# Performance work log

Hardware: AMD Instinct MI355X
Metric: run time of the kernel (lower is better)

The kernel has to match this reference:

```python
import jax, jax.numpy as jnp
import numpy as np

B, H, W = 8, 160, 180
PHASES = 3
DELTA = 0.01
GAMMA = 1.0


def _conv(a, k):
    return jax.lax.conv_general_dilated(a, k, (1, 1), 'SAME',
                                        dimension_numbers=('NCHW', 'OIHW', 'NCHW'))


def _cconv(xr, xi, kr, ki):
    # complex conv via 4 real convs: (xr+i xi) * (kr+i ki)
    return _conv(xr, kr) - _conv(xi, ki), _conv(xr, ki) + _conv(xi, kr)


def _t(k):
    # conv_transpose2d(stride=1, pad=1, 3x3) == conv2d with swapped in/out channels and spatially flipped kernel
    return jnp.flip(jnp.swapaxes(k, 0, 1), axis=(2, 3))


def _cconvT(xr, xi, kr, ki):
    return _cconv(xr, xi, _t(kr), _t(ki))


def _act(x):
    # eq. (33): smoothed ReLU; quadratic inside |x| <= delta
    return jnp.where(jnp.abs(x) > DELTA, jax.nn.relu(x),
                     x * x / (4 * DELTA) + 0.5 * x + DELTA / 4)


def _act_der(x):
    return jnp.where(jnp.abs(x) > DELTA, (x > 0).astype(x.dtype),
                     x / (2 * DELTA) + 0.5)


def _grad_r(xc, convs, thr):
    # gradient of smoothed L2-channel-norm regularizer (grad_r_x1 / grad_r_x2)
    xr = jnp.real(xc).reshape(-1, 1, H, W)
    xi = jnp.imag(xc).reshape(-1, 1, H, W)
    acts = []
    ar, ai = xr, xi
    for kr, ki in convs[:3]:
        pr, pi = _cconv(ar, ai, kr, ki)
        ar, ai = _act(pr), _act(pi)
        acts.append((ar, ai))
    w4r, w4i = _cconv(ar, ai, *convs[3])
    norm = jnp.sqrt(jnp.sum(w4r * w4r + w4i * w4i, axis=1, keepdims=True))
    I1 = (norm > thr).astype(w4r.dtype)
    denom = jnp.maximum(norm, 1e-12)  # F.normalize eps
    gr = I1 * (w4r / denom) + (1 - I1) * (w4r / thr)
    gi = I1 * (w4i / denom) + (1 - I1) * (w4i / thr)
    gr, gi = _cconvT(gr, gi, *convs[3])
    for j in (2, 1, 0):
        # NOTE: faithful to source — derivative evaluated at the ACTIVATED values, complex multiply
        dr, di = _act_der(acts[j][0]), _act_der(acts[j][1])
        gr, gi = gr * dr - gi * di, gr * di + gi * dr
        gr, gi = _cconvT(gr, gi, *convs[j])
    return (gr + 1j * gi).reshape(-1, H, W)


def _grad_f(xc, kc, mask):
    # F^H( M o (M o F x - k) ): mriAdjointOp(mriForwardOp(x,m) - k, m)
    return jnp.fft.ifft2((jnp.fft.fft2(xc) * mask - kc) * mask)


def _forward(x1, x2, k1, k2, mask, convsA, convsB, thr1, thr2, a1, a2, b1, b2):
    to_c = lambda a: a[:, 0] + 1j * a[:, 1]
    x1c, x2c, k1c, k2c = to_c(x1), to_c(x2), to_c(k1), to_c(k2)
    for i in range(PHASES):
        x1c = x1c - a1[i] * _grad_f(x1c, k1c, mask) - b1[i] * _grad_r(x1c, convsA, thr1[0] * GAMMA)
        x2c = x2c - a2[i] * _grad_f(x2c, k2c, mask) - b2[i] * _grad_r(x2c, convsB, thr2[0] * GAMMA)
    return jnp.stack([jnp.real(x1c), jnp.imag(x1c), jnp.real(x2c), jnp.imag(x2c)], axis=1)


def setup_inputs() -> dict:
    key = jax.random.key(0)
    ks = jax.random.split(key, 32)
    d = {}
    d['x1'] = jax.random.normal(ks[0], (B, 2, H, W), jnp.float32)
    d['x2'] = jax.random.normal(ks[1], (B, 2, H, W), jnp.float32)
    d['k1'] = jax.random.normal(ks[2], (B, 2, H, W), jnp.float32)
    d['k2'] = jax.random.normal(ks[3], (B, 2, H, W), jnp.float32)
    d['mask'] = jax.random.uniform(ks[4], (H, W), jnp.float32)
    conv_names = ['conv1r', 'conv1i', 'conv2r', 'conv2i', 'conv3r', 'conv3i', 'conv4r', 'conv4i',
                  'conv1r_', 'conv1i_', 'conv2r_', 'conv2i_', 'conv3r_', 'conv3i_', 'conv4r_', 'conv4i_']
    for j, name in enumerate(conv_names):
        cin = 1 if name.startswith('conv1') else 32
        d[name] = 0.06 * jax.random.normal(ks[5 + j], (32, cin, 3, 3), jnp.float32)  # ~xavier
    d['soft_thr1'] = jnp.full((1,), 0.01, jnp.float32)
    d['soft_thr2'] = jnp.full((1,), 0.01, jnp.float32)
    d['alphas1'] = jnp.full((PHASES,), 0.5, jnp.float32)
    d['alphas2'] = jnp.full((PHASES,), 0.5, jnp.float32)
    d['betas1'] = jnp.full((PHASES,), 0.1, jnp.float32)
    d['betas2'] = jnp.full((PHASES,), 0.1, jnp.float32)
    return d


def reference(x1, x2, k1, k2, mask,
              conv1r, conv1i, conv2r, conv2i, conv3r, conv3i, conv4r, conv4i,
              conv1r_, conv1i_, conv2r_, conv2i_, conv3r_, conv3i_, conv4r_, conv4i_,
              soft_thr1, soft_thr2, alphas1, alphas2, betas1, betas2):
    convsA = [(conv1r, conv1i), (conv2r, conv2i), (conv3r, conv3i), (conv4r, conv4i)]
    convsB = [(conv1r_, conv1i_), (conv2r_, conv2i_), (conv3r_, conv3i_), (conv4r_, conv4i_)]
    return _forward(x1, x2, k1, k2, mask, convsA, convsB,
                    soft_thr1, soft_thr2, alphas1, alphas2, betas1, betas2)
```

## Files before the change

### kernel.cpp

```cpp
#include <hip/hip_runtime.h>
#include <math.h>

#define HH 160
#define WW 180
#define HWSZ (HH*WW)
#define BB 8
#define BB2 16
#define P1 ((size_t)BB*HWSZ)
#define PE2 ((size_t)BB2*32*HWSZ)

typedef unsigned short u16;
typedef unsigned long long ull;
typedef __attribute__((ext_vector_type(8))) short short8;
typedef __attribute__((ext_vector_type(2))) unsigned long long ull2;
typedef __attribute__((ext_vector_type(4))) float floatx4;

struct Ptrs16 { const float* p[16]; };

__device__ __forceinline__ u16 f2b(float f) {
  unsigned u = __builtin_bit_cast(unsigned, f);
  unsigned r = (u + 0x7fffu + ((u >> 16) & 1u)) >> 16;
  return (u16)r;
}
__device__ __forceinline__ float b2f(u16 h) {
  return __builtin_bit_cast(float, ((unsigned)h) << 16);
}

__device__ __forceinline__ float actf(float x) {
  float q = x*x*25.0f + 0.5f*x + 0.0025f;
  float r = fmaxf(x, 0.0f);
  return (fabsf(x) > 0.01f) ? r : q;
}
__device__ __forceinline__ float actdf(float x) {
  float q = x*50.0f + 0.5f;
  float r = (x > 0.0f) ? 1.0f : 0.0f;
  return (fabsf(x) > 0.01f) ? r : q;
}

__global__ void prep_all(Ptrs16 ps, u16* __restrict__ dst0) {
  const int rIdx[12] = {2,4,6,6,4,2,10,12,14,14,12,10};
  const int bwdF[12] = {0,0,0,1,1,1,0,0,0,1,1,1};
  int slot = blockIdx.x / 36;
  int idx = (blockIdx.x % 36)*256 + threadIdx.x;
  if (idx >= 9*32*32) return;
  const float* wr = ps.p[rIdx[slot]];
  const float* wi = ps.p[rIdx[slot]+1];
  u16* dst = dst0 + (size_t)slot*18432;
  int tap = idx >> 10; int rem = idx & 1023; int o = rem >> 5; int c = rem & 31;
  int s = bwdF[slot] ? ((c*32 + o)*9 + (8 - tap)) : ((o*32 + c)*9 + tap);
  float vr = wr[s], vi = wi[s];
  int nt = o >> 4, m = o & 15;
  size_t base = (((size_t)tap*2 + nt)*2*16 + (size_t)m)*32 + c;
  dst[base]       = f2b(vr);
  dst[base + 512] = f2b(vi);
}

template<int MODE>
__global__ __launch_bounds__(256)
void conv_mfma(const u16* __restrict__ inb, const u16* __restrict__ wbA,
               const u16* __restrict__ wbB, u16* __restrict__ outb,
               const u16* __restrict__ derb,
               const float* __restrict__ thrA, const float* __restrict__ thrB)
{
  __shared__ alignas(16) u16 stg[2*6*34*36];
  const int tid = threadIdx.x;
  const int lane = tid & 63, wv = tid >> 6;
  const int x0 = blockIdx.x * 32, y0 = blockIdx.y * 4, b = blockIdx.z;
  const u16* wb = (b < BB) ? wbA : wbB;
  constexpr int PL = 6*34*36;
  const int m = lane & 15, q = lane >> 4;

  for (int j = tid; j < 1632; j += 256) {
    int prow = j / 136; int rem = j - prow*136;
    int col = rem >> 2, chq = rem & 3;
    int plane = prow / 6, row = prow - plane*6;
    int gy = y0 - 1 + row, gx = x0 - 1 + col;
    ull v0 = 0, v1 = 0;
    if (gy >= 0 && gy < HH && gx >= 0 && gx < WW) {
      const ull* src = (const ull*)(inb + (size_t)plane*PE2
                                    + (((size_t)b*HH + gy)*WW + gx)*32 + chq*8);
      v0 = src[0]; v1 = src[1];
    }
    ull* dst = (ull*)&stg[((size_t)prow*34 + col)*36 + chq*8];
    dst[0] = v0; dst[1] = v1;
  }
  __syncthreads();

  floatx4 accr[2][2], acci[2][2];
#pragma unroll
  for (int s = 0; s < 2; ++s)
#pragma unroll
    for (int nt = 0; nt < 2; ++nt) {
      accr[s][nt] = (floatx4){0.f,0.f,0.f,0.f};
      acci[s][nt] = (floatx4){0.f,0.f,0.f,0.f};
    }

#pragma unroll
  for (int tap = 0; tap < 9; ++tap) {
    const int ky = tap / 3, kx = tap - ky*3;
    short8 Pr[2], Pi[2];
#pragma unroll
    for (int s = 0; s < 2; ++s) {
      int cu = ((wv + ky)*34 + (s*16 + m + kx))*36 + q*8;
      const ull* pR = (const ull*)&stg[cu];
      const ull* pI = (const ull*)&stg[cu + PL];
      ull2 vr; vr.x = pR[0]; vr.y = pR[1];
      ull2 vi; vi.x = pI[0]; vi.y = pI[1];
      Pr[s] = __builtin_bit_cast(short8, vr);
      Pi[s] = __builtin_bit_cast(short8, vi);
    }
#pragma unroll
    for (int nt = 0; nt < 2; ++nt) {
      const u16* pw = wb + (size_t)(tap*2 + nt)*1024 + (size_t)m*32 + q*8;
      short8 Wr = *(const short8*)pw;
      short8 Wi = *(const short8*)(pw + 512);
      ull2 wx = __builtin_bit_cast(ull2, Wi);
      wx.x ^= 0x8000800080008000ULL;
      wx.y ^= 0x8000800080008000ULL;
      short8 nWi = __builtin_bit_cast(short8, wx);
#pragma unroll
      for (int s = 0; s < 2; ++s) {
        accr[s][nt] = __builtin_amdgcn_mfma_f32_16x16x32_bf16(Wr,  Pr[s], accr[s][nt], 0, 0, 0);
        accr[s][nt] = __builtin_amdgcn_mfma_f32_16x16x32_bf16(nWi, Pi[s], accr[s][nt], 0, 0, 0);
        acci[s][nt] = __builtin_amdgcn_mfma_f32_16x16x32_bf16(Wr,  Pi[s], acci[s][nt], 0, 0, 0);
        acci[s][nt] = __builtin_amdgcn_mfma_f32_16x16x32_bf16(Wi,  Pr[s], acci[s][nt], 0, 0, 0);
      }
    }
  }

  const int y = y0 + wv;
#pragma unroll
  for (int s = 0; s < 2; ++s) {
    int x = x0 + s*16 + m;
    bool ok = (x < WW);
    float invn = 1.0f;
    if constexpr (MODE == 3) {
      float ss = 0.f;
#pragma unroll
      for (int nt = 0; nt < 2; ++nt)
#pragma unroll
        for (int r = 0; r < 4; ++r)
          ss += accr[s][nt][r]*accr[s][nt][r] + acci[s][nt][r]*acci[s][nt][r];
      ss += __shfl_xor(ss, 16, 64);
      ss += __shfl_xor(ss, 32, 64);
      float thr = (b < BB ? thrA : thrB)[0];
      invn = 1.0f / fmaxf(sqrtf(ss), thr);
    }
    size_t pxbase = (((size_t)b*HH + y)*WW + x)*32;
#pragma unroll
    for (int nt = 0; nt < 2; ++nt) {
      size_t gb = pxbase + nt*16 + q*4;
      ull dR = 0, dI = 0;
      if constexpr (MODE == 2) {
        if (ok) { dR = *(const ull*)(derb + gb); dI = *(const ull*)(derb + PE2 + gb); }
      }
      ull vR = 0, vI = 0;
#pragma unroll
      for (int r = 0; r < 4; ++r) {
        float pr = accr[s][nt][r], pi = acci[s][nt][r];
        if constexpr (MODE == 1) { pr = actf(pr); pi = actf(pi); }
        if constexpr (MODE == 3) { pr *= invn; pi *= invn; }
        if constexpr (MODE == 2) {
          float dr = actdf(b2f((u16)(dR >> (16*r))));
          float di = actdf(b2f((u16)(dI >> (16*r))));
          float nr = pr*dr - pi*di;
          pi = pr*di + pi*dr; pr = nr;
        }
        vR |= (ull)f2b(pr) << (16*r);
        vI |= (ull)f2b(pi) << (16*r);
      }
      if (ok) {
        *(ull*)(outb + gb)       = vR;
        *(ull*)(outb + PE2 + gb) = vI;
      }
    }
  }
}

__global__ __launch_bounds__(256)
void l1fwd(const float* __restrict__ xall,
           const float* __restrict__ wrA, const float* __restrict__ wiA,
           const float* __restrict__ wrB, const float* __restrict__ wiB,
           u16* __restrict__ outb)
{
  __shared__ float hR[10][12], hI[10][12];
  __shared__ float wt[9][32][2];
  const int tid = threadIdx.x;
  const int og = tid & 3, px = tid >> 2;
  const int lx = px & 7, ly = px >> 3;
  const int x0 = blockIdx.x*8, y0 = blockIdx.y*8, b = blockIdx.z;
  const int branch = b >> 3, img = b & 7;
  const float* wr = branch ? wrB : wrA;
  const float* wi = branch ? wiB : wiA;
  const float* xp = xall + (size_t)branch*2*P1 + (size_t)img*HWSZ;

  for (int j = tid; j < 576; j += 256) {
    int tap = j >> 6; int rem = j & 63; int o = rem >> 1, ri = rem & 1;
    wt[tap][o][ri] = ri ? wi[o*9+tap] : wr[o*9+tap];
  }
  for (int j = tid; j < 200; j += 256) {
    int plane = j / 100; int pos = j - plane*100;
    int yy = pos / 10, xx = pos - yy*10;
    int gy = y0 - 1 + yy, gx = x0 - 1 + xx;
    float v = 0.f;
    if (gy >= 0 && gy < HH && gx >= 0 && gx < WW)
      v = xp[(size_t)plane*P1 + (size_t)gy*WW + gx];
    (plane ? hI : hR)[yy][xx] = v;
  }
  __syncthreads();

  float accR[8], accI[8];
#pragma unroll
  for (int o = 0; o < 8; ++o) { accR[o] = 0.f; accI[o] = 0.f; }
#pragma unroll
  for (int tap = 0; tap < 9; ++tap) {
    int ky = tap/3, kx = tap - ky*3;
    float ar = hR[ly+ky][lx+kx], ai = hI[ly+ky][lx+kx];
#pragma unroll
    for (int o = 0; o < 8; ++o) {
      float wrv = wt[tap][og*8+o][0], wiv = wt[tap][og*8+o][1];
      accR[o] += ar*wrv - ai*wiv;
      accI[o] += ar*wiv + ai*wrv;
    }
  }
  int gx = x0 + lx, gy = y0 + ly;
  if (gx < WW) {
    size_t base = (((size_t)b*HH + gy)*WW + gx)*32 + og*8;
    ull* dR = (ull*)(outb + base);
    ull* dI = (ull*)(outb + PE2 + base);
#pragma unroll
    for (int k = 0; k < 2; ++k) {
      ull vR = 0, vI = 0;
#pragma unroll
      for (int t = 0; t < 4; ++t) {
        vR |= (ull)f2b(actf(accR[k*4+t])) << (16*t);
        vI |= (ull)f2b(actf(accI[k*4+t])) << (16*t);
      }
      dR[k] = vR; dI[k] = vI;
    }
  }
}

__global__ __launch_bounds__(256)
void l1bwd(const u16* __restrict__ gb,
           const float* __restrict__ wrA, const float* __restrict__ wiA,
           const float* __restrict__ wrB, const float* __restrict__ wiB,
           float* __restrict__ outp)
{
  __shared__ alignas(16) u16 stg[2*100*32];
  __shared__ float wt[32][9][2];
  const int tid = threadIdx.x;
  const int cg = tid & 3, px = tid >> 2;
  const int lx = px & 7, ly = px >> 3;
  const int x0 = blockIdx.x*8, y0 = blockIdx.y*8, b = blockIdx.z;
  const int branch = b >> 3, img = b & 7;
  const float* wr = branch ? wrB : wrA;
  const float* wi = branch ? wiB : wiA;

  for (int j = tid; j < 576; j += 256) {
    int c = j / 18; int rem = j - c*18; int tap = rem >> 1, ri = rem & 1;
    wt[c][tap][ri] = (ri ? wi : wr)[c*9 + (8-tap)];
  }
  for (int j = tid; j < 800; j += 256) {
    int plane = j / 400; int rem = j - plane*400;
    int pos = rem >> 2, chq = rem & 3;
    int yy = pos / 10, xx = pos - yy*10;
    int gy = y0 - 1 + yy, gx = x0 - 1 + xx;
    ull v0 = 0, v1 = 0;
    if (gy >= 0 && gy < HH && gx >= 0 && gx < WW) {
      const ull* src = (const ull*)(gb + (size_t)plane*PE2
                                    + (((size_t)b*HH + gy)*WW + gx)*32 + chq*8);
      v0 = src[0]; v1 = src[1];
    }
    ull* dst = (ull*)&stg[((size_t)plane*100 + pos)*32 + chq*8];
    dst[0] = v0; dst[1] = v1;
  }
  __syncthreads();

  float gr = 0.f, gi = 0.f;
#pragma unroll
  for (int tap = 0; tap < 9; ++tap) {
    int ky = tap/3, kx = tap - ky*3;
    int pos = (ly+ky)*10 + (lx+kx);
    const ull* pR = (const ull*)&stg[(size_t)pos*32 + cg*8];
    const ull* pI = (const ull*)&stg[(100 + (size_t)pos)*32 + cg*8];
    ull r0 = pR[0], r1 = pR[1], i0 = pI[0], i1 = pI[1];
#pragma unroll
    for (int t = 0; t < 4; ++t) {
      int c = cg*8 + t;
      float ar = b2f((u16)(r0 >> (16*t))), ai = b2f((u16)(i0 >> (16*t)));
      float wrv = wt[c][tap][0], wiv = wt[c][tap][1];
      gr += ar*wrv - ai*wiv;
      gi += ar*wiv + ai*wrv;
    }
#pragma unroll
    for (int t = 0; t < 4; ++t) {
      int c = cg*8 + 4 + t;
      float ar = b2f((u16)(r1 >> (16*t))), ai = b2f((u16)(i1 >> (16*t)));
      float wrv = wt[c][tap][0], wiv = wt[c][tap][1];
      gr += ar*wrv - ai*wiv;
      gi += ar*wiv + ai*wrv;
    }
  }
  gr += __shfl_xor(gr, 1, 64); gr += __shfl_xor(gr, 2, 64);
  gi += __shfl_xor(gi, 1, 64); gi += __shfl_xor(gi, 2, 64);

  int gx = x0 + lx, gy = y0 + ly;
  if (cg == 0 && gx < WW) {
    size_t o2 = (size_t)branch*2*P1 + (size_t)img*HWSZ + (size_t)gy*WW + gx;
    outp[o2]      = gr;
    outp[P1 + o2] = gi;
  }
}

__global__ void gen_dft2(float2* __restrict__ Mf, float2* __restrict__ Mi, int N) {
  int idx = blockIdx.x*256 + threadIdx.x;
  if (idx >= N*N) return;
  int r = idx / N, c = idx - r*N;
  long mm = ((long)r * (long)c) % N;
  double a = 2.0 * 3.14159265358979323846 * (double)mm / (double)N;
  double cs = cos(a), sn = sin(a);
  Mf[idx] = make_float2((float)cs, (float)(-sn));
  Mi[idx] = make_float2((float)(cs/N), (float)(sn/N));
}

__global__ void dft_row_planes(const float* __restrict__ xall,
                               float2* __restrict__ out, const float2* __restrict__ M) {
  int bh = blockIdx.x;
  int v = threadIdx.x; if (v >= WW) return;
  int b2 = bh / HH, h = bh - b2*HH;
  int branch = b2 >> 3, img = b2 & 7;
  const float* rowR = xall + (size_t)branch*2*P1 + (size_t)img*HWSZ + (size_t)h*WW;
  const float* rowI = rowR + P1;
  float ar = 0.f, ai = 0.f;
  for (int w = 0; w < WW; ++w) {
    float sr = rowR[w], si = rowI[w];
    float2 m = M[w*WW + v];
    ar += sr*m.x - si*m.y;
    ai += sr*m.y + si*m.x;
  }
  out[(size_t)bh*WW + v] = make_float2(ar, ai);
}

__global__ void dft_row_c(const float2* __restrict__ in, float2* __restrict__ out,
                          const float2* __restrict__ M) {
  int bh = blockIdx.x;
  int v = threadIdx.x; if (v >= WW) return;
  const float2* row = in + (size_t)bh*WW;
  float ar = 0.f, ai = 0.f;
  for (int w = 0; w < WW; ++w) {
    float2 s = row[w];
    float2 m = M[w*WW + v];
    ar += s.x*m.x - s.y*m.y;
    ai += s.x*m.y + s.y*m.x;
  }
  out[(size_t)bh*WW + v] = make_float2(ar, ai);
}

__global__ void dft_col_c(const float2* __restrict__ in, float2* __restrict__ out,
                          const float2* __restrict__ M) {
  int bu = blockIdx.x;
  int v = threadIdx.x; if (v >= WW) return;
  int b = bu / HH, u = bu - b*HH;
  const float2* base = in + (size_t)b*HWSZ;
  float ar = 0.f, ai = 0.f;
  for (int h = 0; h < HH; ++h) {
    float2 m = M[u*HH + h];
    float2 s = base[(size_t)h*WW + v];
    ar += s.x*m.x - s.y*m.y;
    ai += s.x*m.y + s.y*m.x;
  }
  out[(size_t)bu*WW + v] = make_float2(ar, ai);
}

__global__ void dft_col_mask(const float2* __restrict__ in, float2* __restrict__ out,
                             const float2* __restrict__ M, const float* __restrict__ mask) {
  int bu = blockIdx.x;
  int v = threadIdx.x; if (v >= WW) return;
  int b = bu / HH, u = bu - b*HH;
  const float2* base = in + (size_t)b*HWSZ;
  float ar = 0.f, ai = 0.f;
  for (int h = 0; h < HH; ++h) {
    float mk = mask[h*WW + v]; float mm = mk*mk;
    float2 m = M[u*HH + h];
    float2 s = base[(size_t)h*WW + v];
    float sr = s.x*mm, si = s.y*mm;
    ar += sr*m.x - si*m.y;
    ai += sr*m.y + si*m.x;
  }
  out[(size_t)bu*WW + v] = make_float2(ar, ai);
}

__global__ void dft_row_update(const float2* __restrict__ in, const float2* __restrict__ M,
                               const float2* __restrict__ ctall, const float* __restrict__ grp,
                               float* __restrict__ xall,
                               const float* __restrict__ al1, const float* __restrict__ al2,
                               const float* __restrict__ be1, const float* __restrict__ be2,
                               int phase) {
  int bh = blockIdx.x;
  int v = threadIdx.x; if (v >= WW) return;
  int b2 = bh / HH, h = bh - b2*HH;
  int branch = b2 >> 3, img = b2 & 7;
  const float2* row = in + (size_t)bh*WW;
  float ar = 0.f, ai = 0.f;
  for (int w = 0; w < WW; ++w) {
    float2 s = row[w];
    float2 m = M[w*WW + v];
    ar += s.x*m.x - s.y*m.y;
    ai += s.x*m.y + s.y*m.x;
  }
  float2 ct = ctall[(size_t)bh*WW + v];
  float a   = (branch ? al2 : al1)[phase];
  float bet = (branch ? be2 : be1)[phase];
  size_t xo = (size_t)branch*2*P1 + (size_t)img*HWSZ + (size_t)h*WW + v;
  xall[xo]      -= a*(ar - ct.x) + bet*grp[xo];
  xall[P1 + xo] -= a*(ai - ct.y) + bet*grp[P1 + xo];
}

__global__ void maskk_m(const float* __restrict__ k1, const float* __restrict__ k2,
                        const float* __restrict__ mask, float2* __restrict__ t) {
  int i = blockIdx.x*256 + threadIdx.x;
  if (i >= (int)(2*P1)) return;
  int branch = i >= (int)P1;
  int ii = i - branch*(int)P1;
  int b = ii / HWSZ, p = ii - b*HWSZ;
  const float* k = branch ? k2 : k1;
  float m = mask[p];
  t[i] = make_float2(m * k[(size_t)b*2*HWSZ + p], m * k[(size_t)b*2*HWSZ + HWSZ + p]);
}

__global__ void unpack_m(const float* __restrict__ x1, const float* __restrict__ x2,
                         float* __restrict__ xall) {
  int i = blockIdx.x*256 + threadIdx.x;
  if (i >= (int)(2*P1)) return;
  int branch = i >= (int)P1;
  int ii = i - branch*(int)P1;
  int b = ii / HWSZ, p = ii - b*HWSZ;
  const float* src = branch ? x2 : x1;
  size_t dst = (size_t)branch*2*P1 + (size_t)b*HWSZ + p;
  xall[dst]      = src[(size_t)b*2*HWSZ + p];
  xall[P1 + dst] = src[(size_t)b*2*HWSZ + HWSZ + p];
}

__global__ void pack_kernel(const float* __restrict__ xall, float* __restrict__ out) {
  int i = blockIdx.x*256 + threadIdx.x;
  if (i >= (int)P1) return;
  int b = i / HWSZ, p = i - b*HWSZ;
  size_t ob = (size_t)b*4*HWSZ;
  size_t x1o = (size_t)b*HWSZ + p;
  size_t x2o = 2*P1 + x1o;
  out[ob + p]          = xall[x1o];
  out[ob + HWSZ + p]   = xall[P1 + x1o];
  out[ob + 2*HWSZ + p] = xall[x2o];
  out[ob + 3*HWSZ + p] = xall[P1 + x2o];
}

extern "C" void kernel_launch(void* const* d_in, const int* in_sizes, int n_in,
                              void* d_out, int out_size, void* d_ws, size_t ws_size,
                              hipStream_t stream) {
  (void)in_sizes; (void)n_in; (void)out_size; (void)ws_size;
  const float* x1in = (const float*)d_in[0];
  const float* x2in = (const float*)d_in[1];
  const float* k1   = (const float*)d_in[2];
  const float* k2   = (const float*)d_in[3];
  const float* mask = (const float*)d_in[4];
  Ptrs16 cw;
  for (int i = 0; i < 16; ++i) cw.p[i] = (const float*)d_in[5+i];
  const float* thr1 = (const float*)d_in[21];
  const float* thr2 = (const float*)d_in[22];
  const float* al1  = (const float*)d_in[23];
  const float* al2  = (const float*)d_in[24];
  const float* be1  = (const float*)d_in[25];
  const float* be2  = (const float*)d_in[26];
  float* out = (float*)d_out;

  u16* U = (u16*)d_ws;
  size_t uoff = 0;
  auto alloc_u = [&](size_t n){ u16* p = U + uoff; uoff += (n + 15) & ~(size_t)15; return p; };
  u16* act1 = alloc_u(2*PE2);
  u16* act2 = alloc_u(2*PE2);
  u16* act3 = alloc_u(2*PE2);
  u16* w4b  = alloc_u(2*PE2);
  u16* wp0  = alloc_u(12*18432);

  float* F = (float*)(U + uoff);
  size_t off = 0;
  auto alloc_f = [&](size_t n){ float* p = F + off; off += (n + 3) & ~(size_t)3; return p; };
  float*  xall = alloc_f(4*P1);
  float*  grp  = alloc_f(4*P1);
  float2* t1   = (float2*)alloc_f(4*P1);
  float2* t2   = (float2*)alloc_f(4*P1);
  float2* ctall= (float2*)alloc_f(4*P1);
  float2* EWf  = (float2*)alloc_f(2*(size_t)WW*WW);
  float2* EWi  = (float2*)alloc_f(2*(size_t)WW*WW);
  float2* EHf  = (float2*)alloc_f(2*(size_t)HH*HH);
  float2* EHi  = (float2*)alloc_f(2*(size_t)HH*HH);

  const dim3 MG(6, 40, BB2);
  const dim3 LG(23, 20, BB2);
  const int NP1 = (int)((P1 + 255)/256);
  const int NP2 = (int)((2*P1 + 255)/256);
  const int DFTG = BB2*HH;
  const int DFTB = 192;

  gen_dft2<<<(WW*WW+255)/256, 256, 0, stream>>>(EWf, EWi, WW);
  gen_dft2<<<(HH*HH+255)/256, 256, 0, stream>>>(EHf, EHi, HH);
  prep_all<<<12*36, 256, 0, stream>>>(cw, wp0);
  unpack_m<<<NP2, 256, 0, stream>>>(x1in, x2in, xall);

  maskk_m<<<NP2, 256, 0, stream>>>(k1, k2, mask, t1);
  dft_col_c<<<DFTG, DFTB, 0, stream>>>(t1, t2, EHi);
  dft_row_c<<<DFTG, DFTB, 0, stream>>>(t2, ctall, EWi);

  u16* WA[6]; u16* WB[6];
  for (int i = 0; i < 6; ++i) { WA[i] = wp0 + (size_t)i*18432; WB[i] = wp0 + (size_t)(6+i)*18432; }

  for (int ph = 0; ph < 3; ++ph) {
    l1fwd<<<LG, 256, 0, stream>>>(xall, cw.p[0], cw.p[1], cw.p[8], cw.p[9], act1);
    conv_mfma<1><<<MG, 256, 0, stream>>>(act1, WA[0], WB[0], act2, nullptr, nullptr, nullptr);
    conv_mfma<1><<<MG, 256, 0, stream>>>(act2, WA[1], WB[1], act3, nullptr, nullptr, nullptr);
    conv_mfma<3><<<MG, 256, 0, stream>>>(act3, WA[2], WB[2], w4b, nullptr, thr1, thr2);
    conv_mfma<2><<<MG, 256, 0, stream>>>(w4b,  WA[3], WB[3], act3, act3, nullptr, nullptr);
    conv_mfma<2><<<MG, 256, 0, stream>>>(act3, WA[4], WB[4], act2, act2, nullptr, nullptr);
    conv_mfma<2><<<MG, 256, 0, stream>>>(act2, WA[5], WB[5], act1, act1, nullptr, nullptr);
    l1bwd<<<LG, 256, 0, stream>>>(act1, cw.p[0], cw.p[1], cw.p[8], cw.p[9], grp);
    dft_row_planes<<<DFTG, DFTB, 0, stream>>>(xall, t1, EWf);
    dft_col_c<<<DFTG, DFTB, 0, stream>>>(t1, t2, EHf);
    dft_col_mask<<<DFTG, DFTB, 0, stream>>>(t2, t1, EHi, mask);
    dft_row_update<<<DFTG, DFTB, 0, stream>>>(t1, EWi, ctall, grp, xall,
                                              al1, al2, be1, be2, ph);
  }

  pack_kernel<<<NP1, 256, 0, stream>>>(xall, out);
}
```

Before: 2.005 ms.

## Make conv_mfma blocks loop over five row tiles with double-buffered LDS staging

Each conv_mfma block now handles 20 rows (five 4-row tiles) instead of 4. The next tile's input halo is prefetched into registers while the current tile's MFMAs run, then written to a second LDS buffer. This is meant to hide global-load latency behind compute and to amortize address setup and the weight-pointer choice across tiles. In exchange LDS use doubles, register pressure rises from the 14 prefetched 64-bit values, and the grid shrinks fivefold (6x8x16 blocks), which may leave the GPU underfilled.

```diff
diff --git a/kernel.cpp b/kernel.cpp
--- a/kernel.cpp
+++ b/kernel.cpp
@@ -62,117 +62,158 @@
                const u16* __restrict__ derb,
                const float* __restrict__ thrA, const float* __restrict__ thrB)
 {
-  __shared__ alignas(16) u16 stg[2*6*34*36];
+  constexpr int PL = 6*34*36;
+  constexpr int PB = 2*PL;
+  __shared__ alignas(16) u16 stg[2*PB];
   const int tid = threadIdx.x;
   const int lane = tid & 63, wv = tid >> 6;
-  const int x0 = blockIdx.x * 32, y0 = blockIdx.y * 4, b = blockIdx.z;
+  const int x0 = blockIdx.x * 32;
+  const int yb = blockIdx.y * 20;
+  const int b  = blockIdx.z;
   const u16* wb = (b < BB) ? wbA : wbB;
-  constexpr int PL = 6*34*36;
   const int m = lane & 15, q = lane >> 4;
 
-  for (int j = tid; j < 1632; j += 256) {
-    int prow = j / 136; int rem = j - prow*136;
-    int col = rem >> 2, chq = rem & 3;
-    int plane = prow / 6, row = prow - plane*6;
-    int gy = y0 - 1 + row, gx = x0 - 1 + col;
-    ull v0 = 0, v1 = 0;
-    if (gy >= 0 && gy < HH && gx >= 0 && gx < WW) {
-      const ull* src = (const ull*)(inb + (size_t)plane*PE2
-                                    + (((size_t)b*HH + gy)*WW + gx)*32 + chq*8);
-      v0 = src[0]; v1 = src[1];
-    }
-    ull* dst = (ull*)&stg[((size_t)prow*34 + col)*36 + chq*8];
-    dst[0] = v0; dst[1] = v1;
-  }
-  __syncthreads();
-
-  floatx4 accr[2][2], acci[2][2];
-#pragma unroll
-  for (int s = 0; s < 2; ++s)
-#pragma unroll
-    for (int nt = 0; nt < 2; ++nt) {
-      accr[s][nt] = (floatx4){0.f,0.f,0.f,0.f};
-      acci[s][nt] = (floatx4){0.f,0.f,0.f,0.f};
-    }
-
-#pragma unroll
-  for (int tap = 0; tap < 9; ++tap) {
-    const int ky = tap / 3, kx = tap - ky*3;
-    short8 Pr[2], Pi[2];
+  const u16* srcp[7]; int ldso[7]; int rowa[7]; bool act[7]; bool wok[7];
+#pragma unroll
+  for (int k = 0; k < 7; ++k) {
+    int j = tid + k*256;
+    bool inr = (j < 1632);
+    int jj = inr ? j : 0;
+    int chq = jj & 3; int r2 = jj >> 2;
+    int col = r2 % 34; int pr = r2 / 34;
+    int row = pr % 6;  int plane = pr / 6;
+    int gx = x0 - 1 + col;
+    bool gxok = (gx >= 0) && (gx < WW);
+    srcp[k] = inb + (size_t)plane*PE2
+            + (((size_t)b*HH + (yb - 1 + row))*WW + gx)*32 + chq*8;
+    ldso[k] = (pr*34 + col)*36 + chq*8;
+    rowa[k] = yb - 1 + row;
+    act[k]  = inr && gxok;
+    wok[k]  = inr;
+  }
+  const size_t YSTRIDE = (size_t)4*WW*32;
+
+  ull vreg[14];
+  auto stage_regs = [&](int t) {
+#pragma unroll
+    for (int k = 0; k < 7; ++k) {
+      int gy = rowa[k] + 4*t;
+      bool ok = act[k] && (gy >= 0) && (gy < HH);
+      const ull* sp = (const ull*)(srcp[k] + (size_t)t*YSTRIDE);
+      vreg[2*k]   = ok ? sp[0] : 0;
+      vreg[2*k+1] = ok ? sp[1] : 0;
+    }
+  };
+  auto write_lds = [&](int buf) {
+    u16* base = &stg[buf*PB];
+#pragma unroll
+    for (int k = 0; k < 7; ++k) {
+      if (wok[k]) {
+        ull* dp = (ull*)&base[ldso[k]];
+        dp[0] = vreg[2*k]; dp[1] = vreg[2*k+1];
+      }
+    }
+  };
+
+  stage_regs(0); write_lds(0); __syncthreads();
+
+  for (int t = 0; t < 5; ++t) {
+    if (t < 4) stage_regs(t + 1);
+
+    const u16* sb = &stg[(t & 1)*PB];
+    floatx4 accr[2][2], acci[2][2];
+#pragma unroll
+    for (int s = 0; s < 2; ++s)
+#pragma unroll
+      for (int nt = 0; nt < 2; ++nt) {
+        accr[s][nt] = (floatx4){0.f,0.f,0.f,0.f};
+        acci[s][nt] = (floatx4){0.f,0.f,0.f,0.f};
+      }
+
+#pragma unroll
+    for (int tap = 0; tap < 9; ++tap) {
+      const int ky = tap / 3, kx = tap - ky*3;
+      short8 Pr[2], Pi[2];
+#pragma unroll
+      for (int s = 0; s < 2; ++s) {
+        int cu = ((wv + ky)*34 + (s*16 + m + kx))*36 + q*8;
+        const ull* pR = (const ull*)&sb[cu];
+        const ull* pI = (const ull*)&sb[cu + PL];
+        ull2 vr; vr.x = pR[0]; vr.y = pR[1];
+        ull2 vi; vi.x = pI[0]; vi.y = pI[1];
+        Pr[s] = __builtin_bit_cast(short8, vr);
+        Pi[s] = __builtin_bit_cast(short8, vi);
+      }
+#pragma unroll
+      for (int nt = 0; nt < 2; ++nt) {
+        const u16* pw = wb + (size_t)(tap*2 + nt)*1024 + (size_t)m*32 + q*8;
+        short8 Wr = *(const short8*)pw;
+        short8 Wi = *(const short8*)(pw + 512);
+        ull2 wx = __builtin_bit_cast(ull2, Wi);
+        wx.x ^= 0x8000800080008000ULL;
+        wx.y ^= 0x8000800080008000ULL;
+        short8 nWi = __builtin_bit_cast(short8, wx);
+#pragma unroll
+        for (int s = 0; s < 2; ++s) {
+          accr[s][nt] = __builtin_amdgcn_mfma_f32_16x16x32_bf16(Wr,  Pr[s], accr[s][nt], 0, 0, 0);
+          accr[s][nt] = __builtin_amdgcn_mfma_f32_16x16x32_bf16(nWi, Pi[s], accr[s][nt], 0, 0, 0);
+          acci[s][nt] = __builtin_amdgcn_mfma_f32_16x16x32_bf16(Wr,  Pi[s], acci[s][nt], 0, 0, 0);
+          acci[s][nt] = __builtin_amdgcn_mfma_f32_16x16x32_bf16(Wi,  Pr[s], acci[s][nt], 0, 0, 0);
+        }
+      }
+    }
+
+    const int y = yb + t*4 + wv;
 #pragma unroll
     for (int s = 0; s < 2; ++s) {
-      int cu = ((wv + ky)*34 + (s*16 + m + kx))*36 + q*8;
-      const ull* pR = (const ull*)&stg[cu];
-      const ull* pI = (const ull*)&stg[cu + PL];
-      ull2 vr; vr.x = pR[0]; vr.y = pR[1];
-      ull2 vi; vi.x = pI[0]; vi.y = pI[1];
-      Pr[s] = __builtin_bit_cast(short8, vr);
-      Pi[s] = __builtin_bit_cast(short8, vi);
-    }
-#pragma unroll
-    for (int nt = 0; nt < 2; ++nt) {
-      const u16* pw = wb + (size_t)(tap*2 + nt)*1024 + (size_t)m*32 + q*8;
-      short8 Wr = *(const short8*)pw;
-      short8 Wi = *(const short8*)(pw + 512);
-      ull2 wx = __builtin_bit_cast(ull2, Wi);
-      wx.x ^= 0x8000800080008000ULL;
-      wx.y ^= 0x8000800080008000ULL;
-      short8 nWi = __builtin_bit_cast(short8, wx);
-#pragma unroll
-      for (int s = 0; s < 2; ++s) {
-        accr[s][nt] = __builtin_amdgcn_mfma_f32_16x16x32_bf16(Wr,  Pr[s], accr[s][nt], 0, 0, 0);
-        accr[s][nt] = __builtin_amdgcn_mfma_f32_16x16x32_bf16(nWi, Pi[s], accr[s][nt], 0, 0, 0);
-        acci[s][nt] = __builtin_amdgcn_mfma_f32_16x16x32_bf16(Wr,  Pi[s], acci[s][nt], 0, 0, 0);
-        acci[s][nt] = __builtin_amdgcn_mfma_f32_16x16x32_bf16(Wi,  Pr[s], acci[s][nt], 0, 0, 0);
-      }
-    }
-  }
-
-  const int y = y0 + wv;
-#pragma unroll
-  for (int s = 0; s < 2; ++s) {
-    int x = x0 + s*16 + m;
-    bool ok = (x < WW);
-    float invn = 1.0f;
-    if constexpr (MODE == 3) {
-      float ss = 0.f;
-#pragma unroll
-      for (int nt = 0; nt < 2; ++nt)
-#pragma unroll
-        for (int r = 0; r < 4; ++r)
-          ss += accr[s][nt][r]*accr[s][nt][r] + acci[s][nt][r]*acci[s][nt][r];
-      ss += __shfl_xor(ss, 16, 64);
-      ss += __shfl_xor(ss, 32, 64);
-      float thr = (b < BB ? thrA : thrB)[0];
-      invn = 1.0f / fmaxf(sqrtf(ss), thr);
-    }
-    size_t pxbase = (((size_t)b*HH + y)*WW + x)*32;
-#pragma unroll
-    for (int nt = 0; nt < 2; ++nt) {
-      size_t gb = pxbase + nt*16 + q*4;
-      ull dR = 0, dI = 0;
-      if constexpr (MODE == 2) {
-        if (ok) { dR = *(const ull*)(derb + gb); dI = *(const ull*)(derb + PE2 + gb); }
-      }
-      ull vR = 0, vI = 0;
-#pragma unroll
-      for (int r = 0; r < 4; ++r) {
-        float pr = accr[s][nt][r], pi = acci[s][nt][r];
-        if constexpr (MODE == 1) { pr = actf(pr); pi = actf(pi); }
-        if constexpr (MODE == 3) { pr *= invn; pi *= invn; }
+      int x = x0 + s*16 + m;
+      bool ok = (x < WW);
+      float invn = 1.0f;
+      if constexpr (MODE == 3) {
+        float ss = 0.f;
+#pragma unroll
+        for (int nt = 0; nt < 2; ++nt)
+#pragma unroll
+          for (int r = 0; r < 4; ++r)
+            ss += accr[s][nt][r]*accr[s][nt][r] + acci[s][nt][r]*acci[s][nt][r];
+        ss += __shfl_xor(ss, 16, 64);
+        ss += __shfl_xor(ss, 32, 64);
+        float thr = (b < BB ? thrA : thrB)[0];
+        invn = 1.0f / fmaxf(sqrtf(ss), thr);
+      }
+      size_t pxbase = (((size_t)b*HH + y)*WW + x)*32;
+#pragma unroll
+      for (int nt = 0; nt < 2; ++nt) {
+        size_t gb = pxbase + nt*16 + q*4;
+        ull dR = 0, dI = 0;
         if constexpr (MODE == 2) {
-          float dr = actdf(b2f((u16)(dR >> (16*r))));
-          float di = actdf(b2f((u16)(dI >> (16*r))));
-          float nr = pr*dr - pi*di;
-          pi = pr*di + pi*dr; pr = nr;
+          if (ok) { dR = *(const ull*)(derb + gb); dI = *(const ull*)(derb + PE2 + gb); }
         }
-        vR |= (ull)f2b(pr) << (16*r);
-        vI |= (ull)f2b(pi) << (16*r);
-      }
-      if (ok) {
-        *(ull*)(outb + gb)       = vR;
-        *(ull*)(outb + PE2 + gb) = vI;
-      }
+        ull vR = 0, vI = 0;
+#pragma unroll
+        for (int r = 0; r < 4; ++r) {
+          float pr = accr[s][nt][r], pi = acci[s][nt][r];
+          if constexpr (MODE == 1) { pr = actf(pr); pi = actf(pi); }
+          if constexpr (MODE == 3) { pr *= invn; pi *= invn; }
+          if constexpr (MODE == 2) {
+            float dr = actdf(b2f((u16)(dR >> (16*r))));
+            float di = actdf(b2f((u16)(dI >> (16*r))));
+            float nr = pr*dr - pi*di;
+            pi = pr*di + pi*dr; pr = nr;
+          }
+          vR |= (ull)f2b(pr) << (16*r);
+          vI |= (ull)f2b(pi) << (16*r);
+        }
+        if (ok) {
+          *(ull*)(outb + gb)       = vR;
+          *(ull*)(outb + PE2 + gb) = vI;
+        }
+      }
+    }
+
+    if (t < 4) {
+      write_lds((t + 1) & 1);
+      __syncthreads();
     }
   }
 }
@@ -496,7 +537,7 @@
   float2* EHf  = (float2*)alloc_f(2*(size_t)HH*HH);
   float2* EHi  = (float2*)alloc_f(2*(size_t)HH*HH);
 
-  const dim3 MG(6, 40, BB2);
+  const dim3 MG(6, 8, BB2);
   const dim3 LG(23, 20, BB2);
   const int NP1 = (int)((P1 + 255)/256);
   const int NP2 = (int)((2*P1 + 255)/256);
```

After: 2.035 ms. No clear change (+1.5%).

## Overlap DFT data-consistency work with conv kernels via extra blocks; merge setup kernels

Applied to the files above, without the earlier changes.

The forward row DFT now runs as extra thread blocks inside the first conv launch, and the column DFT, mask and inverse column DFT run as extra blocks inside the second conv launch, using shared memory for a whole image column. The DFT path no longer waits behind the regularizer convs, and three launches per phase are removed. The setup kernels (DFT matrix generation, weight prep, unpack, mask·k) are merged into one launch. The cost is longer conv launches with mixed block types. The fused column DFT also drops the strided global reads of the old separate kernels.

```diff
diff --git a/kernel.cpp b/kernel.cpp
--- a/kernel.cpp
+++ b/kernel.cpp
@@ -9,6 +9,8 @@
 #define P1 ((size_t)BB*HWSZ)
 #define PE2 ((size_t)BB2*32*HWSZ)
 
+#define NCONV 3840
+
 typedef unsigned short u16;
 typedef unsigned long long ull;
 typedef __attribute__((ext_vector_type(8))) short short8;
@@ -37,35 +39,136 @@
   return (fabsf(x) > 0.01f) ? r : q;
 }
 
-__global__ void prep_all(Ptrs16 ps, u16* __restrict__ dst0) {
-  const int rIdx[12] = {2,4,6,6,4,2,10,12,14,14,12,10};
-  const int bwdF[12] = {0,0,0,1,1,1,0,0,0,1,1,1};
-  int slot = blockIdx.x / 36;
-  int idx = (blockIdx.x % 36)*256 + threadIdx.x;
-  if (idx >= 9*32*32) return;
-  const float* wr = ps.p[rIdx[slot]];
-  const float* wi = ps.p[rIdx[slot]+1];
-  u16* dst = dst0 + (size_t)slot*18432;
-  int tap = idx >> 10; int rem = idx & 1023; int o = rem >> 5; int c = rem & 31;
-  int s = bwdF[slot] ? ((c*32 + o)*9 + (8 - tap)) : ((o*32 + c)*9 + tap);
-  float vr = wr[s], vi = wi[s];
-  int nt = o >> 4, m = o & 15;
-  size_t base = (((size_t)tap*2 + nt)*2*16 + (size_t)m)*32 + c;
-  dst[base]       = f2b(vr);
-  dst[base + 512] = f2b(vi);
-}
-
-template<int MODE>
+__global__ __launch_bounds__(256)
+void setup_all(Ptrs16 ps, u16* __restrict__ wp0,
+               const float* __restrict__ x1, const float* __restrict__ x2,
+               float* __restrict__ xall,
+               const float* __restrict__ k1, const float* __restrict__ k2,
+               const float* __restrict__ mask, float2* __restrict__ t1,
+               float2* __restrict__ EWf, float2* __restrict__ EWi,
+               float2* __restrict__ EHf, float2* __restrict__ EHi)
+{
+  const int id = blockIdx.x, tid = threadIdx.x;
+  if (id < 127) {
+    int idx = id*256 + tid; if (idx >= WW*WW) return;
+    int r = idx / WW, c = idx - r*WW;
+    long mm = ((long)r * (long)c) % WW;
+    double a = 2.0 * 3.14159265358979323846 * (double)mm / (double)WW;
+    double cs = cos(a), sn = sin(a);
+    EWf[idx] = make_float2((float)cs, (float)(-sn));
+    EWi[idx] = make_float2((float)(cs/WW), (float)(sn/WW));
+  } else if (id < 227) {
+    int idx = (id-127)*256 + tid; if (idx >= HH*HH) return;
+    int r = idx / HH, c = idx - r*HH;
+    long mm = ((long)r * (long)c) % HH;
+    double a = 2.0 * 3.14159265358979323846 * (double)mm / (double)HH;
+    double cs = cos(a), sn = sin(a);
+    EHf[idx] = make_float2((float)cs, (float)(-sn));
+    EHi[idx] = make_float2((float)(cs/HH), (float)(sn/HH));
+  } else if (id < 659) {
+    const int rIdx[12] = {2,4,6,6,4,2,10,12,14,14,12,10};
+    const int bwdF[12] = {0,0,0,1,1,1,0,0,0,1,1,1};
+    int pb = id - 227;
+    int slot = pb / 36;
+    int idx = (pb % 36)*256 + tid;
+    if (idx >= 9*32*32) return;
+    const float* wr = ps.p[rIdx[slot]];
+    const float* wi = ps.p[rIdx[slot]+1];
+    u16* dst = wp0 + (size_t)slot*18432;
+    int tap = idx >> 10; int rem = idx & 1023; int o = rem >> 5; int c = rem & 31;
+    int s = bwdF[slot] ? ((c*32 + o)*9 + (8 - tap)) : ((o*32 + c)*9 + tap);
+    int nt = o >> 4, m = o & 15;
+    size_t base = (((size_t)tap*2 + nt)*2*16 + (size_t)m)*32 + c;
+    dst[base]       = f2b(wr[s]);
+    dst[base + 512] = f2b(wi[s]);
+  } else if (id < 2459) {
+    int i = (id-659)*256 + tid; if (i >= (int)(2*P1)) return;
+    int branch = i >= (int)P1;
+    int ii = i - branch*(int)P1;
+    int b = ii / HWSZ, p = ii - b*HWSZ;
+    const float* src = branch ? x2 : x1;
+    size_t dst = (size_t)branch*2*P1 + (size_t)b*HWSZ + p;
+    xall[dst]      = src[(size_t)b*2*HWSZ + p];
+    xall[P1 + dst] = src[(size_t)b*2*HWSZ + HWSZ + p];
+  } else {
+    int i = (id-2459)*256 + tid; if (i >= (int)(2*P1)) return;
+    int branch = i >= (int)P1;
+    int ii = i - branch*(int)P1;
+    int b = ii / HWSZ, p = ii - b*HWSZ;
+    const float* k = branch ? k2 : k1;
+    float m = mask[p];
+    t1[i] = make_float2(m * k[(size_t)b*2*HWSZ + p], m * k[(size_t)b*2*HWSZ + HWSZ + p]);
+  }
+}
+
+template<int MODE, int EXTRA>
 __global__ __launch_bounds__(256)
 void conv_mfma(const u16* __restrict__ inb, const u16* __restrict__ wbA,
                const u16* __restrict__ wbB, u16* __restrict__ outb,
                const u16* __restrict__ derb,
-               const float* __restrict__ thrA, const float* __restrict__ thrB)
+               const float* __restrict__ thrA, const float* __restrict__ thrB,
+               const float* __restrict__ xall, float2* __restrict__ t1,
+               const float2* __restrict__ EWf, const float2* __restrict__ EHf,
+               const float2* __restrict__ EHi, const float* __restrict__ mask)
 {
   __shared__ alignas(16) u16 stg[2*6*34*36];
-  const int tid = threadIdx.x;
+  const int id = blockIdx.x, tid = threadIdx.x;
+
+  if (EXTRA == 1 && id >= NCONV) {
+    int j = id - NCONV;
+    int v = tid; if (v >= WW) return;
+    int b2 = j / HH, h = j - b2*HH;
+    int branch = b2 >> 3, img = b2 & 7;
+    const float* rowR = xall + (size_t)branch*2*P1 + (size_t)img*HWSZ + (size_t)h*WW;
+    const float* rowI = rowR + P1;
+    float ar = 0.f, ai = 0.f;
+    for (int w = 0; w < WW; ++w) {
+      float sr = rowR[w], si = rowI[w];
+      float2 m = EWf[w*WW + v];
+      ar += sr*m.x - si*m.y;
+      ai += sr*m.y + si*m.x;
+    }
+    t1[(size_t)j*WW + v] = make_float2(ar, ai);
+    return;
+  }
+  if (EXTRA == 2 && id >= NCONV) {
+    int j = id - NCONV;
+    int b = j / WW, v = j - b*WW;
+    float2* cbA = (float2*)stg;
+    float2* cbB = ((float2*)stg) + HH;
+    if (tid < HH) cbA[tid] = t1[((size_t)(b*HH) + tid)*WW + v];
+    __syncthreads();
+    if (tid < HH) {
+      int u = tid;
+      float ar = 0.f, ai = 0.f;
+      for (int h = 0; h < HH; ++h) {
+        float2 m = EHf[u*HH + h];
+        float2 s = cbA[h];
+        ar += s.x*m.x - s.y*m.y;
+        ai += s.x*m.y + s.y*m.x;
+      }
+      float mk = mask[u*WW + v]; float mm = mk*mk;
+      cbB[u] = make_float2(ar*mm, ai*mm);
+    }
+    __syncthreads();
+    if (tid < HH) {
+      int u2 = tid;
+      float ar = 0.f, ai = 0.f;
+      for (int u = 0; u < HH; ++u) {
+        float2 m = EHi[u2*HH + u];
+        float2 s = cbB[u];
+        ar += s.x*m.x - s.y*m.y;
+        ai += s.x*m.y + s.y*m.x;
+      }
+      t1[((size_t)(b*HH) + u2)*WW + v] = make_float2(ar, ai);
+    }
+    return;
+  }
+
   const int lane = tid & 63, wv = tid >> 6;
-  const int x0 = blockIdx.x * 32, y0 = blockIdx.y * 4, b = blockIdx.z;
+  const int x0 = (id % 6) * 32;
+  const int y0 = ((id / 6) % 40) * 4;
+  const int b  = id / 240;
   const u16* wb = (b < BB) ? wbA : wbB;
   constexpr int PL = 6*34*36;
   const int m = lane & 15, q = lane >> 4;
@@ -313,50 +416,6 @@
   }
 }
 
-__global__ void gen_dft2(float2* __restrict__ Mf, float2* __restrict__ Mi, int N) {
-  int idx = blockIdx.x*256 + threadIdx.x;
-  if (idx >= N*N) return;
-  int r = idx / N, c = idx - r*N;
-  long mm = ((long)r * (long)c) % N;
-  double a = 2.0 * 3.14159265358979323846 * (double)mm / (double)N;
-  double cs = cos(a), sn = sin(a);
-  Mf[idx] = make_float2((float)cs, (float)(-sn));
-  Mi[idx] = make_float2((float)(cs/N), (float)(sn/N));
-}
-
-__global__ void dft_row_planes(const float* __restrict__ xall,
-                               float2* __restrict__ out, const float2* __restrict__ M) {
-  int bh = blockIdx.x;
-  int v = threadIdx.x; if (v >= WW) return;
-  int b2 = bh / HH, h = bh - b2*HH;
-  int branch = b2 >> 3, img = b2 & 7;
-  const float* rowR = xall + (size_t)branch*2*P1 + (size_t)img*HWSZ + (size_t)h*WW;
-  const float* rowI = rowR + P1;
-  float ar = 0.f, ai = 0.f;
-  for (int w = 0; w < WW; ++w) {
-    float sr = rowR[w], si = rowI[w];
-    float2 m = M[w*WW + v];
-    ar += sr*m.x - si*m.y;
-    ai += sr*m.y + si*m.x;
-  }
-  out[(size_t)bh*WW + v] = make_float2(ar, ai);
-}
-
-__global__ void dft_row_c(const float2* __restrict__ in, float2* __restrict__ out,
-                          const float2* __restrict__ M) {
-  int bh = blockIdx.x;
-  int v = threadIdx.x; if (v >= WW) return;
-  const float2* row = in + (size_t)bh*WW;
-  float ar = 0.f, ai = 0.f;
-  for (int w = 0; w < WW; ++w) {
-    float2 s = row[w];
-    float2 m = M[w*WW + v];
-    ar += s.x*m.x - s.y*m.y;
-    ai += s.x*m.y + s.y*m.x;
-  }
-  out[(size_t)bh*WW + v] = make_float2(ar, ai);
-}
-
 __global__ void dft_col_c(const float2* __restrict__ in, float2* __restrict__ out,
                           const float2* __restrict__ M) {
   int bu = blockIdx.x;
@@ -373,22 +432,19 @@
   out[(size_t)bu*WW + v] = make_float2(ar, ai);
 }
 
-__global__ void dft_col_mask(const float2* __restrict__ in, float2* __restrict__ out,
-                             const float2* __restrict__ M, const float* __restrict__ mask) {
-  int bu = blockIdx.x;
+__global__ void dft_row_c(const float2* __restrict__ in, float2* __restrict__ out,
+                          const float2* __restrict__ M) {
+  int bh = blockIdx.x;
   int v = threadIdx.x; if (v >= WW) return;
-  int b = bu / HH, u = bu - b*HH;
-  const float2* base = in + (size_t)b*HWSZ;
+  const float2* row = in + (size_t)bh*WW;
   float ar = 0.f, ai = 0.f;
-  for (int h = 0; h < HH; ++h) {
-    float mk = mask[h*WW + v]; float mm = mk*mk;
-    float2 m = M[u*HH + h];
-    float2 s = base[(size_t)h*WW + v];
-    float sr = s.x*mm, si = s.y*mm;
-    ar += sr*m.x - si*m.y;
-    ai += sr*m.y + si*m.x;
-  }
-  out[(size_t)bu*WW + v] = make_float2(ar, ai);
+  for (int w = 0; w < WW; ++w) {
+    float2 s = row[w];
+    float2 m = M[w*WW + v];
+    ar += s.x*m.x - s.y*m.y;
+    ai += s.x*m.y + s.y*m.x;
+  }
+  out[(size_t)bh*WW + v] = make_float2(ar, ai);
 }
 
 __global__ void dft_row_update(const float2* __restrict__ in, const float2* __restrict__ M,
@@ -415,31 +471,6 @@
   size_t xo = (size_t)branch*2*P1 + (size_t)img*HWSZ + (size_t)h*WW + v;
   xall[xo]      -= a*(ar - ct.x) + bet*grp[xo];
   xall[P1 + xo] -= a*(ai - ct.y) + bet*grp[P1 + xo];
-}
-
-__global__ void maskk_m(const float* __restrict__ k1, const float* __restrict__ k2,
-                        const float* __restrict__ mask, float2* __restrict__ t) {
-  int i = blockIdx.x*256 + threadIdx.x;
-  if (i >= (int)(2*P1)) return;
-  int branch = i >= (int)P1;
-  int ii = i - branch*(int)P1;
-  int b = ii / HWSZ, p = ii - b*HWSZ;
-  const float* k = branch ? k2 : k1;
-  float m = mask[p];
-  t[i] = make_float2(m * k[(size_t)b*2*HWSZ + p], m * k[(size_t)b*2*HWSZ + HWSZ + p]);
-}
-
-__global__ void unpack_m(const float* __restrict__ x1, const float* __restrict__ x2,
-                         float* __restrict__ xall) {
-  int i = blockIdx.x*256 + threadIdx.x;
-  if (i >= (int)(2*P1)) return;
-  int branch = i >= (int)P1;
-  int ii = i - branch*(int)P1;
-  int b = ii / HWSZ, p = ii - b*HWSZ;
-  const float* src = branch ? x2 : x1;
-  size_t dst = (size_t)branch*2*P1 + (size_t)b*HWSZ + p;
-  xall[dst]      = src[(size_t)b*2*HWSZ + p];
-  xall[P1 + dst] = src[(size_t)b*2*HWSZ + HWSZ + p];
 }
 
 __global__ void pack_kernel(const float* __restrict__ xall, float* __restrict__ out) {
@@ -496,19 +527,13 @@
   float2* EHf  = (float2*)alloc_f(2*(size_t)HH*HH);
   float2* EHi  = (float2*)alloc_f(2*(size_t)HH*HH);
 
-  const dim3 MG(6, 40, BB2);
   const dim3 LG(23, 20, BB2);
   const int NP1 = (int)((P1 + 255)/256);
-  const int NP2 = (int)((2*P1 + 255)/256);
   const int DFTG = BB2*HH;
   const int DFTB = 192;
 
-  gen_dft2<<<(WW*WW+255)/256, 256, 0, stream>>>(EWf, EWi, WW);
-  gen_dft2<<<(HH*HH+255)/256, 256, 0, stream>>>(EHf, EHi, HH);
-  prep_all<<<12*36, 256, 0, stream>>>(cw, wp0);
-  unpack_m<<<NP2, 256, 0, stream>>>(x1in, x2in, xall);
-
-  maskk_m<<<NP2, 256, 0, stream>>>(k1, k2, mask, t1);
+  setup_all<<<4259, 256, 0, stream>>>(cw, wp0, x1in, x2in, xall, k1, k2, mask, t1,
+                                      EWf, EWi, EHf, EHi);
   dft_col_c<<<DFTG, DFTB, 0, stream>>>(t1, t2, EHi);
   dft_row_c<<<DFTG, DFTB, 0, stream>>>(t2, ctall, EWi);
 
@@ -517,16 +542,19 @@
 
   for (int ph = 0; ph < 3; ++ph) {
     l1fwd<<<LG, 256, 0, stream>>>(xall, cw.p[0], cw.p[1], cw.p[8], cw.p[9], act1);
-    conv_mfma<1><<<MG, 256, 0, stream>>>(act1, WA[0], WB[0], act2, nullptr, nullptr, nullptr);
-    conv_mfma<1><<<MG, 256, 0, stream>>>(act2, WA[1], WB[1], act3, nullptr, nullptr, nullptr);
-    conv_mfma<3><<<MG, 256, 0, stream>>>(act3, WA[2], WB[2], w4b, nullptr, thr1, thr2);
-    conv_mfma<2><<<MG, 256, 0, stream>>>(w4b,  WA[3], WB[3], act3, act3, nullptr, nullptr);
-    conv_mfma<2><<<MG, 256, 0, stream>>>(act3, WA[4], WB[4], act2, act2, nullptr, nullptr);
-    conv_mfma<2><<<MG, 256, 0, stream>>>(act2, WA[5], WB[5], act1, act1, nullptr, nullptr);
+    conv_mfma<1,1><<<NCONV + 2560, 256, 0, stream>>>(act1, WA[0], WB[0], act2, nullptr,
+        nullptr, nullptr, xall, t1, EWf, EHf, EHi, mask);
+    conv_mfma<1,2><<<NCONV + BB2*WW, 256, 0, stream>>>(act2, WA[1], WB[1], act3, nullptr,
+        nullptr, nullptr, xall, t1, EWf, EHf, EHi, mask);
+    conv_mfma<3,0><<<NCONV, 256, 0, stream>>>(act3, WA[2], WB[2], w4b, nullptr,
+        thr1, thr2, xall, t1, EWf, EHf, EHi, mask);
+    conv_mfma<2,0><<<NCONV, 256, 0, stream>>>(w4b,  WA[3], WB[3], act3, act3,
+        nullptr, nullptr, xall, t1, EWf, EHf, EHi, mask);
+    conv_mfma<2,0><<<NCONV, 256, 0, stream>>>(act3, WA[4], WB[4], act2, act2,
+        nullptr, nullptr, xall, t1, EWf, EHf, EHi, mask);
+    conv_mfma<2,0><<<NCONV, 256, 0, stream>>>(act2, WA[5], WB[5], act1, act1,
+        nullptr, nullptr, xall, t1, EWf, EHf, EHi, mask);
     l1bwd<<<LG, 256, 0, stream>>>(act1, cw.p[0], cw.p[1], cw.p[8], cw.p[9], grp);
-    dft_row_planes<<<DFTG, DFTB, 0, stream>>>(xall, t1, EWf);
-    dft_col_c<<<DFTG, DFTB, 0, stream>>>(t1, t2, EHf);
-    dft_col_mask<<<DFTG, DFTB, 0, stream>>>(t2, t1, EHi, mask);
     dft_row_update<<<DFTG, DFTB, 0, stream>>>(t1, EWi, ctall, grp, xall,
                                               al1, al2, be1, be2, ph);
   }
```

Result: slower. 2.157 ms (+7.6%).
